# Kernel tuning notes

Measured on AMD Instinct MI355X. Metric: run time of the kernel, lower is better.

The kernel has to match this reference:

```python
import jax, jax.numpy as jnp
import numpy as np

EMBED_DIM = 1024
NUM_HEADS = 16
HEAD_DIM = EMBED_DIM // NUM_HEADS


def setup_inputs() -> dict:
    key = jax.random.key(0)
    ks = jax.random.split(key, 9)
    B, S, D = 2, 2048, EMBED_DIM
    scale = 1.0 / np.sqrt(D)
    inp = {
        "x": jax.random.normal(ks[0], (B, S, D), dtype=jnp.float32),
        "w_q": jax.random.normal(ks[1], (D, D), dtype=jnp.float32) * scale,
        "b_q": jnp.zeros((D,), dtype=jnp.float32),
        "w_k": jax.random.normal(ks[2], (D, D), dtype=jnp.float32) * scale,
        "b_k": jnp.zeros((D,), dtype=jnp.float32),
        "w_v": jax.random.normal(ks[3], (D, D), dtype=jnp.float32) * scale,
        "b_v": jnp.zeros((D,), dtype=jnp.float32),
        "w_o": jax.random.normal(ks[4], (D, D), dtype=jnp.float32) * scale,
        "b_o": jnp.zeros((D,), dtype=jnp.float32),
    }
    return inp


def reference(x, w_q, b_q, w_k, b_k, w_v, b_v, w_o, b_o):
    B, S, D = x.shape
    H, Hd = NUM_HEADS, HEAD_DIM

    def proj(w, b):
        # (B,S,D) @ (D,D) -> (B,S,D) -> (B,H,S,Hd)
        y = jnp.einsum('bsd,df->bsf', x, w) + b
        return y.reshape(B, S, H, Hd).transpose(0, 2, 1, 3)

    q = proj(w_q, b_q)
    k = proj(w_k, b_k)
    v = proj(w_v, b_v)

    scores = jnp.einsum('bhqd,bhkd->bhqk', q, k) / jnp.sqrt(jnp.float32(Hd))
    attn = jax.nn.softmax(scores, axis=-1)
    context = jnp.einsum('bhqk,bhkd->bhqd', attn, v)
    context = context.transpose(0, 2, 1, 3).reshape(B, S, D)
    return jnp.einsum('bsd,df->bsf', context + x, w_o) + b_o
```

## Files before the change

kernel.cpp:

```cpp
#include <hip/hip_runtime.h>
#include <hip/hip_bf16.h>

typedef _Float16 f16;
typedef _Float16 f16x8 __attribute__((ext_vector_type(8)));
typedef _Float16 f16x4 __attribute__((ext_vector_type(4)));
typedef float f32x4 __attribute__((ext_vector_type(4)));

#define EMBED 1024
#define NHEAD 16
#define HDIM 64
#define SEQ 2048
#define BATCH 2
#define NROW (BATCH * SEQ)
#define PSTR 72
#define WBYTES (2 * 64 * PSTR * 2)
#define MBIAS 14.4269504089f
#define QSCALE 0.1803368801f

__device__ __forceinline__ void gld_lds16(const f16* g, f16* l) {
    __builtin_amdgcn_global_load_lds(
        (const __attribute__((address_space(1))) void*)g,
        (__attribute__((address_space(3))) void*)l, 16, 0, 0);
}

__global__ void k_prep(const float* __restrict__ wq, const float* __restrict__ wk,
                       const float* __restrict__ wv, const float* __restrict__ wo,
                       const float* __restrict__ x,
                       f16* __restrict__ wqkvt, f16* __restrict__ wot, f16* __restrict__ xb) {
    if (blockIdx.z >= 4) {
        int i = (((blockIdx.z - 4) * 1024 + blockIdx.y * 32 + blockIdx.x) * 256 + threadIdx.x) * 4;
        float4 v = *(const float4*)&x[i];
        f16x4 o = {(f16)v.x, (f16)v.y, (f16)v.z, (f16)v.w};
        *(f16x4*)&xb[i] = o;
        return;
    }
    const float* W;
    f16* Wt;
    switch (blockIdx.z) {
        case 0: W = wq; Wt = wqkvt; break;
        case 1: W = wk; Wt = wqkvt + 1024 * 1024; break;
        case 2: W = wv; Wt = wqkvt + 2 * 1024 * 1024; break;
        default: W = wo; Wt = wot; break;
    }
    __shared__ float t[32][33];
    int tx = threadIdx.x & 31, ty = threadIdx.x >> 5;
    int r0 = blockIdx.y * 32, c0 = blockIdx.x * 32;
    for (int j = 0; j < 4; ++j)
        t[ty + j * 8][tx] = W[(r0 + ty + j * 8) * 1024 + c0 + tx];
    __syncthreads();
    for (int j = 0; j < 4; ++j)
        Wt[(c0 + ty + j * 8) * 1024 + r0 + tx] = (f16)t[tx][ty + j * 8];
}

__global__ void k_bias(const float* __restrict__ bq, const float* __restrict__ bk,
                       const float* __restrict__ bv, float* __restrict__ bias) {
    int i = blockIdx.x * blockDim.x + threadIdx.x;
    if (i < 3072) bias[i] = (i < 1024) ? bq[i] : ((i < 2048) ? bk[i - 1024] : bv[i - 2048]);
}

template <bool SWAP>
__device__ __forceinline__ void gemm_kloop(const f16* __restrict__ A, const f16* __restrict__ Bt,
                                           int K, f16* Al, f16* Bl, int m0, int n0,
                                           int w, int quad, int l16, int mw, int nw,
                                           int crow, int ccol, f32x4 (&acc)[4][4]) {
    for (int k0 = 0; k0 < K; k0 += 32) {
        __syncthreads();
        gld_lds16(&A[(m0 + crow) * K + k0 + ccol], &Al[(w * 64) * 8]);
        gld_lds16(&A[(m0 + 64 + crow) * K + k0 + ccol], &Al[(256 + w * 64) * 8]);
        gld_lds16(&Bt[(n0 + crow) * K + k0 + ccol], &Bl[(w * 64) * 8]);
        gld_lds16(&Bt[(n0 + 64 + crow) * K + k0 + ccol], &Bl[(256 + w * 64) * 8]);
        __syncthreads();
        f16x8 af[4], bf[4];
        for (int i = 0; i < 4; ++i)
            af[i] = *(const f16x8*)&Al[(mw + i * 16 + l16) * 32 + quad * 8];
        for (int j = 0; j < 4; ++j)
            bf[j] = *(const f16x8*)&Bl[(nw + j * 16 + l16) * 32 + quad * 8];
        for (int i = 0; i < 4; ++i)
            for (int j = 0; j < 4; ++j)
                acc[i][j] = SWAP
                    ? __builtin_amdgcn_mfma_f32_16x16x32_f16(bf[j], af[i], acc[i][j], 0, 0, 0)
                    : __builtin_amdgcn_mfma_f32_16x16x32_f16(af[i], bf[j], acc[i][j], 0, 0, 0);
    }
}

__global__ __launch_bounds__(256) void k_gemm_qkv(const f16* __restrict__ A, const f16* __restrict__ Bt,
                                                  const float* __restrict__ bias,
                                                  f16* __restrict__ qk, f16* __restrict__ Vt) {
    __shared__ __align__(16) f16 Al[128 * 32];
    __shared__ __align__(16) f16 Bl[128 * 32];
    const int K = 1024;
    int tid = threadIdx.x;
    int w = tid >> 6, lane = tid & 63, quad = lane >> 4, l16 = lane & 15;
    int m0 = blockIdx.x * 128, n0 = blockIdx.y * 128;
    int mw = (w >> 1) * 64, nw = (w & 1) * 64;
    int c = w * 64 + lane;
    int crow = c >> 2, ccol = (c & 3) * 8;
    f32x4 acc[4][4] = {};

    if (n0 >= 2048) {
        gemm_kloop<true>(A, Bt, K, Al, Bl, m0, n0, w, quad, l16, mw, nw, crow, ccol, acc);
        for (int i = 0; i < 4; ++i) {
            int mrow = m0 + mw + i * 16 + l16;
            int b = mrow >> 11, s = mrow & 2047;
            for (int j = 0; j < 4; ++j)
                for (int r = 0; r < 4; ++r) {
                    int col = n0 + nw + j * 16 + quad * 4 + r;
                    int d = col - 2048;
                    Vt[(b * 1024 + d) * SEQ + s] = (f16)(acc[i][j][r] + bias[col]);
                }
        }
    } else {
        gemm_kloop<false>(A, Bt, K, Al, Bl, m0, n0, w, quad, l16, mw, nw, crow, ccol, acc);
        for (int i = 0; i < 4; ++i) {
            int row = m0 + mw + i * 16 + quad * 4;
            for (int j = 0; j < 4; ++j) {
                int col = n0 + nw + j * 16 + l16;
                float bval = bias[col];
                for (int r = 0; r < 4; ++r)
                    qk[(row + r) * 2048 + col] = (f16)(acc[i][j][r] + bval);
            }
        }
    }
}

__global__ __launch_bounds__(256) void k_gemm_out(const f16* __restrict__ A, const f16* __restrict__ Bt,
                                                  const float* __restrict__ bias, float* __restrict__ Cout) {
    __shared__ __align__(16) f16 Al[128 * 32];
    __shared__ __align__(16) f16 Bl[64 * 32];
    const int K = 1024, N = 1024;
    int tid = threadIdx.x;
    int w = tid >> 6, lane = tid & 63, quad = lane >> 4, l16 = lane & 15;
    int m0 = blockIdx.x * 128, n0 = blockIdx.y * 64;
    int mw = (w >> 1) * 64, nw = (w & 1) * 32;
    int c = w * 64 + lane;
    int crow = c >> 2, ccol = (c & 3) * 8;
    f32x4 acc[4][2] = {};

    for (int k0 = 0; k0 < K; k0 += 32) {
        __syncthreads();
        gld_lds16(&A[(m0 + crow) * K + k0 + ccol], &Al[(w * 64) * 8]);
        gld_lds16(&A[(m0 + 64 + crow) * K + k0 + ccol], &Al[(256 + w * 64) * 8]);
        gld_lds16(&Bt[(n0 + crow) * K + k0 + ccol], &Bl[(w * 64) * 8]);
        __syncthreads();
        f16x8 af[4], bf[2];
        for (int i = 0; i < 4; ++i)
            af[i] = *(const f16x8*)&Al[(mw + i * 16 + l16) * 32 + quad * 8];
        for (int j = 0; j < 2; ++j)
            bf[j] = *(const f16x8*)&Bl[(nw + j * 16 + l16) * 32 + quad * 8];
        for (int i = 0; i < 4; ++i)
            for (int j = 0; j < 2; ++j)
                acc[i][j] = __builtin_amdgcn_mfma_f32_16x16x32_f16(af[i], bf[j], acc[i][j], 0, 0, 0);
    }

    for (int i = 0; i < 4; ++i) {
        int row = m0 + mw + i * 16 + quad * 4;
        for (int j = 0; j < 2; ++j) {
            int col = n0 + nw + j * 16 + l16;
            float bval = bias[col];
            for (int r = 0; r < 4; ++r)
                Cout[(row + r) * N + col] = acc[i][j][r] + bval;
        }
    }
}

__global__ __launch_bounds__(256, 2) void k_attn(const f16* __restrict__ qk, const f16* __restrict__ Vt,
                                                 const float* __restrict__ x, f16* __restrict__ ctx) {
    __shared__ __align__(16) char smem[4 * WBYTES];

    int tid = threadIdx.x;
    int w = tid >> 6, lane = tid & 63, quad = lane >> 4, l16 = lane & 15;
    int q0 = blockIdx.x * 64;
    int bh = blockIdx.y, b = bh >> 4, h = bh & 15;
    int kbase = 1024 + h * 64;
    int qcol = h * 64;
    int vbase = b * 1024 + h * 64;

    f16* Kw = (f16*)(smem + w * WBYTES);
    f16* Vw = Kw + 64 * PSTR;
    f16* Pw = Kw;

    f16x8 qf[4][2];
    for (int qg = 0; qg < 4; ++qg) {
        int qrow = b * SEQ + q0 + qg * 16 + l16;
        for (int kk = 0; kk < 2; ++kk) {
            f16x8 v = *(const f16x8*)&qk[qrow * 2048 + qcol + kk * 32 + quad * 8];
            for (int e = 0; e < 8; ++e) v[e] = (f16)((float)v[e] * QSCALE);
            qf[qg][kk] = v;
        }
    }

    int srow = lane >> 3;
    int scol = (lane & 7) * 8;
    const f16* kgp = &qk[(b * SEQ + w * 512 + srow) * 2048 + kbase + scol];
    const f16* vgp = &Vt[(vbase + srow) * SEQ + w * 512 + scol];

    f32x4 oacc[4][4] = {};
    float li[4] = {0.f, 0.f, 0.f, 0.f};

    for (int kt = 0; kt < 8; ++kt) {
        f16x8 tk[8], tv[8];
        for (int c = 0; c < 8; ++c) {
            tk[c] = *(const f16x8*)(kgp + c * 8 * 2048);
            tv[c] = *(const f16x8*)(vgp + c * 8 * SEQ);
        }
        kgp += 64 * 2048;
        vgp += 64;
        for (int c = 0; c < 8; ++c) {
            *(f16x8*)&Kw[(c * 8 + srow) * PSTR + scol] = tk[c];
            *(f16x8*)&Vw[(c * 8 + srow) * PSTR + scol] = tv[c];
        }

        f16x8 kf[4][2];
        for (int nt = 0; nt < 4; ++nt)
            for (int kk = 0; kk < 2; ++kk)
                kf[nt][kk] = *(const f16x8*)&Kw[(nt * 16 + l16) * PSTR + kk * 32 + quad * 8];
        asm volatile("s_waitcnt lgkmcnt(0)" ::: "memory");

        for (int qg = 0; qg < 4; ++qg) {
            f32x4 st[4];
            for (int nt = 0; nt < 4; ++nt) {
                f32x4 s = {};
                s = __builtin_amdgcn_mfma_f32_16x16x32_f16(kf[nt][0], qf[qg][0], s, 0, 0, 0);
                s = __builtin_amdgcn_mfma_f32_16x16x32_f16(kf[nt][1], qf[qg][1], s, 0, 0, 0);
                st[nt] = s;
            }
            float rs = 0.f;
            for (int nt = 0; nt < 4; ++nt)
                for (int r = 0; r < 4; ++r) {
                    float p = __builtin_amdgcn_exp2f(st[nt][r] - MBIAS);
                    st[nt][r] = p;
                    rs += p;
                }
            rs += __shfl_xor(rs, 16);
            rs += __shfl_xor(rs, 32);
            li[qg] += rs;
            for (int nt = 0; nt < 4; ++nt) {
                f16x4 pk;
                for (int r = 0; r < 4; ++r) pk[r] = (f16)st[nt][r];
                *(f16x4*)&Pw[(qg * 16 + l16) * PSTR + nt * 16 + quad * 4] = pk;
            }
        }
        asm volatile("s_waitcnt lgkmcnt(0)" ::: "memory");

        f16x8 pf[4][2];
        for (int qg = 0; qg < 4; ++qg)
            for (int kk = 0; kk < 2; ++kk)
                pf[qg][kk] = *(const f16x8*)&Pw[(qg * 16 + l16) * PSTR + kk * 32 + quad * 8];
        for (int nt = 0; nt < 4; ++nt) {
            f16x8 vf0 = *(const f16x8*)&Vw[(nt * 16 + l16) * PSTR + quad * 8];
            f16x8 vf1 = *(const f16x8*)&Vw[(nt * 16 + l16) * PSTR + 32 + quad * 8];
            for (int qg = 0; qg < 4; ++qg) {
                oacc[qg][nt] = __builtin_amdgcn_mfma_f32_16x16x32_f16(pf[qg][0], vf0, oacc[qg][nt], 0, 0, 0);
                oacc[qg][nt] = __builtin_amdgcn_mfma_f32_16x16x32_f16(pf[qg][1], vf1, oacc[qg][nt], 0, 0, 0);
            }
        }
    }

    __syncthreads();
    float* Ow = (float*)(smem + w * WBYTES);
    float* Lw = (float*)(smem + w * WBYTES + 16384);
    for (int qg = 0; qg < 4; ++qg)
        for (int nt = 0; nt < 4; ++nt)
            for (int r = 0; r < 4; ++r)
                Ow[(qg * 16 + quad * 4 + r) * 64 + nt * 16 + l16] = oacc[qg][nt][r];
    if (quad == 0)
        for (int qg = 0; qg < 4; ++qg) Lw[qg * 16 + l16] = li[qg];
    __syncthreads();

    int q = tid >> 2, d0 = (tid & 3) * 16;
    f32x4 a4[4] = {};
    float lsum = 0.f;
    for (int w2 = 0; w2 < 4; ++w2) {
        const float* Ow2 = (const float*)(smem + w2 * WBYTES);
        const float* Lw2 = (const float*)(smem + w2 * WBYTES + 16384);
        for (int j = 0; j < 4; ++j)
            a4[j] += *(const f32x4*)&Ow2[q * 64 + d0 + 4 * j];
        lsum += Lw2[q];
    }
    int g = b * SEQ + q0 + q;
    int cb = h * 64 + d0;
    float inv = 1.f / lsum;
    f16x8 o0, o1;
    for (int j = 0; j < 4; ++j) {
        float4 xv = *(const float4*)&x[g * 1024 + cb + 4 * j];
        float4 r;
        r.x = a4[j][0] * inv + xv.x;
        r.y = a4[j][1] * inv + xv.y;
        r.z = a4[j][2] * inv + xv.z;
        r.w = a4[j][3] * inv + xv.w;
        f16* dst = (j < 2) ? (f16*)&o0 : (f16*)&o1;
        int o = (j & 1) * 4;
        dst[o + 0] = (f16)r.x; dst[o + 1] = (f16)r.y; dst[o + 2] = (f16)r.z; dst[o + 3] = (f16)r.w;
    }
    *(f16x8*)&ctx[g * 1024 + cb] = o0;
    *(f16x8*)&ctx[g * 1024 + cb + 8] = o1;
}

extern "C" void kernel_launch(void* const* d_in, const int* in_sizes, int n_in,
                              void* d_out, int out_size, void* d_ws, size_t ws_size,
                              hipStream_t stream) {
    const float* x  = (const float*)d_in[0];
    const float* wq = (const float*)d_in[1];
    const float* bq = (const float*)d_in[2];
    const float* wk = (const float*)d_in[3];
    const float* bk = (const float*)d_in[4];
    const float* wv = (const float*)d_in[5];
    const float* bv = (const float*)d_in[6];
    const float* wo = (const float*)d_in[7];
    const float* bo = (const float*)d_in[8];
    float* out = (float*)d_out;

    char* ws = (char*)d_ws;
    f16*   xb    = (f16*)(ws);
    f16*   wqkvt = (f16*)(ws + (8u << 20));
    f16*   wot   = (f16*)(ws + (14u << 20));
    float* biasq = (float*)(ws + (16u << 20));
    f16*   qkbuf = (f16*)(ws + (16u << 20) + (64u << 10));
    f16*   vtbuf = (f16*)(ws + (32u << 20) + (64u << 10));
    f16*   ctx   = xb;

    k_prep<<<dim3(32, 32, 8), 256, 0, stream>>>(wq, wk, wv, wo, x, wqkvt, wot, xb);
    k_bias<<<12, 256, 0, stream>>>(bq, bk, bv, biasq);

    k_gemm_qkv<<<dim3(32, 24), 256, 0, stream>>>(xb, wqkvt, biasq, qkbuf, vtbuf);
    k_attn<<<dim3(SEQ / 64, BATCH * NHEAD), 256, 0, stream>>>(qkbuf, vtbuf, x, ctx);
    k_gemm_out<<<dim3(32, 16), 256, 0, stream>>>(ctx, wot, bo, out);
}
```

Baseline: 214.2 us.

## Load K/V MFMA fragments directly from global, shrink LDS, raise occupancy

Stops staging K and V tiles through per-wave LDS buffers and reads the MFMA operand fragments straight from global memory, so LDS holds only the P tile. The smaller LDS footprint lets launch bounds rise from 2 to 4 blocks per CU. The final cross-wave reduction is reworked to fit the smaller buffer: two waves write partial outputs and row sums, then the other two add theirs in after a barrier. Direct fragment loads are less coalesced (16-byte pieces spread across rows) and rely on the cache, and the reduction now needs an extra barrier.

```diff
diff --git a/kernel.cpp b/kernel.cpp
--- a/kernel.cpp
+++ b/kernel.cpp
@@ -13,7 +13,7 @@
 #define BATCH 2
 #define NROW (BATCH * SEQ)
 #define PSTR 72
-#define WBYTES (2 * 64 * PSTR * 2)
+#define PBYTES (64 * PSTR * 2)
 #define MBIAS 14.4269504089f
 #define QSCALE 0.1803368801f
 
@@ -163,9 +163,9 @@
     }
 }
 
-__global__ __launch_bounds__(256, 2) void k_attn(const f16* __restrict__ qk, const f16* __restrict__ Vt,
+__global__ __launch_bounds__(256, 4) void k_attn(const f16* __restrict__ qk, const f16* __restrict__ Vt,
                                                  const float* __restrict__ x, f16* __restrict__ ctx) {
-    __shared__ __align__(16) char smem[4 * WBYTES];
+    __shared__ __align__(16) char smem[4 * PBYTES];
 
     int tid = threadIdx.x;
     int w = tid >> 6, lane = tid & 63, quad = lane >> 4, l16 = lane & 15;
@@ -175,9 +175,7 @@
     int qcol = h * 64;
     int vbase = b * 1024 + h * 64;
 
-    f16* Kw = (f16*)(smem + w * WBYTES);
-    f16* Vw = Kw + 64 * PSTR;
-    f16* Pw = Kw;
+    f16* Pw = (f16*)(smem + w * PBYTES);
 
     f16x8 qf[4][2];
     for (int qg = 0; qg < 4; ++qg) {
@@ -189,32 +187,19 @@
         }
     }
 
-    int srow = lane >> 3;
-    int scol = (lane & 7) * 8;
-    const f16* kgp = &qk[(b * SEQ + w * 512 + srow) * 2048 + kbase + scol];
-    const f16* vgp = &Vt[(vbase + srow) * SEQ + w * 512 + scol];
+    const f16* kfp = &qk[(b * SEQ + w * 512 + l16) * 2048 + kbase + quad * 8];
+    const f16* vfp = &Vt[(vbase + l16) * SEQ + w * 512 + quad * 8];
 
     f32x4 oacc[4][4] = {};
     float li[4] = {0.f, 0.f, 0.f, 0.f};
 
     for (int kt = 0; kt < 8; ++kt) {
-        f16x8 tk[8], tv[8];
-        for (int c = 0; c < 8; ++c) {
-            tk[c] = *(const f16x8*)(kgp + c * 8 * 2048);
-            tv[c] = *(const f16x8*)(vgp + c * 8 * SEQ);
-        }
-        kgp += 64 * 2048;
-        vgp += 64;
-        for (int c = 0; c < 8; ++c) {
-            *(f16x8*)&Kw[(c * 8 + srow) * PSTR + scol] = tk[c];
-            *(f16x8*)&Vw[(c * 8 + srow) * PSTR + scol] = tv[c];
-        }
-
         f16x8 kf[4][2];
-        for (int nt = 0; nt < 4; ++nt)
-            for (int kk = 0; kk < 2; ++kk)
-                kf[nt][kk] = *(const f16x8*)&Kw[(nt * 16 + l16) * PSTR + kk * 32 + quad * 8];
-        asm volatile("s_waitcnt lgkmcnt(0)" ::: "memory");
+        for (int nt = 0; nt < 4; ++nt) {
+            kf[nt][0] = *(const f16x8*)(kfp + nt * 16 * 2048);
+            kf[nt][1] = *(const f16x8*)(kfp + nt * 16 * 2048 + 32);
+        }
+        kfp += 64 * 2048;
 
         for (int qg = 0; qg < 4; ++qg) {
             f32x4 st[4];
@@ -247,36 +232,48 @@
             for (int kk = 0; kk < 2; ++kk)
                 pf[qg][kk] = *(const f16x8*)&Pw[(qg * 16 + l16) * PSTR + kk * 32 + quad * 8];
         for (int nt = 0; nt < 4; ++nt) {
-            f16x8 vf0 = *(const f16x8*)&Vw[(nt * 16 + l16) * PSTR + quad * 8];
-            f16x8 vf1 = *(const f16x8*)&Vw[(nt * 16 + l16) * PSTR + 32 + quad * 8];
+            f16x8 vf0 = *(const f16x8*)(vfp + nt * 16 * SEQ);
+            f16x8 vf1 = *(const f16x8*)(vfp + nt * 16 * SEQ + 32);
             for (int qg = 0; qg < 4; ++qg) {
                 oacc[qg][nt] = __builtin_amdgcn_mfma_f32_16x16x32_f16(pf[qg][0], vf0, oacc[qg][nt], 0, 0, 0);
                 oacc[qg][nt] = __builtin_amdgcn_mfma_f32_16x16x32_f16(pf[qg][1], vf1, oacc[qg][nt], 0, 0, 0);
             }
         }
-    }
-
+        vfp += 64;
+    }
+
+    float* Ow = (float*)(smem + (w & 1) * 16640);
+    float* Lw = (float*)(smem + (w & 1) * 16640 + 16384);
     __syncthreads();
-    float* Ow = (float*)(smem + w * WBYTES);
-    float* Lw = (float*)(smem + w * WBYTES + 16384);
-    for (int qg = 0; qg < 4; ++qg)
-        for (int nt = 0; nt < 4; ++nt)
-            for (int r = 0; r < 4; ++r)
-                Ow[(qg * 16 + quad * 4 + r) * 64 + nt * 16 + l16] = oacc[qg][nt][r];
-    if (quad == 0)
-        for (int qg = 0; qg < 4; ++qg) Lw[qg * 16 + l16] = li[qg];
+    if (w < 2) {
+        for (int qg = 0; qg < 4; ++qg)
+            for (int nt = 0; nt < 4; ++nt)
+                for (int r = 0; r < 4; ++r)
+                    Ow[(qg * 16 + quad * 4 + r) * 64 + nt * 16 + l16] = oacc[qg][nt][r];
+        if (quad == 0)
+            for (int qg = 0; qg < 4; ++qg) Lw[qg * 16 + l16] = li[qg];
+    }
     __syncthreads();
+    if (w >= 2) {
+        for (int qg = 0; qg < 4; ++qg)
+            for (int nt = 0; nt < 4; ++nt)
+                for (int r = 0; r < 4; ++r)
+                    Ow[(qg * 16 + quad * 4 + r) * 64 + nt * 16 + l16] += oacc[qg][nt][r];
+        if (quad == 0)
+            for (int qg = 0; qg < 4; ++qg) Lw[qg * 16 + l16] += li[qg];
+    }
+    __syncthreads();
 
     int q = tid >> 2, d0 = (tid & 3) * 16;
-    f32x4 a4[4] = {};
-    float lsum = 0.f;
-    for (int w2 = 0; w2 < 4; ++w2) {
-        const float* Ow2 = (const float*)(smem + w2 * WBYTES);
-        const float* Lw2 = (const float*)(smem + w2 * WBYTES + 16384);
-        for (int j = 0; j < 4; ++j)
-            a4[j] += *(const f32x4*)&Ow2[q * 64 + d0 + 4 * j];
-        lsum += Lw2[q];
-    }
+    const float* O0 = (const float*)smem;
+    const float* O1 = (const float*)(smem + 16640);
+    f32x4 a4[4];
+    for (int j = 0; j < 4; ++j)
+        a4[j] = *(const f32x4*)&O0[q * 64 + d0 + 4 * j];
+    for (int j = 0; j < 4; ++j)
+        a4[j] += *(const f32x4*)&O1[q * 64 + d0 + 4 * j];
+    float lsum = ((const float*)(smem + 16384))[q] + ((const float*)(smem + 16640 + 16384))[q];
+
     int g = b * SEQ + q0 + q;
     int cb = h * 64 + d0;
     float inv = 1.f / lsum;
```

After: 332.5 us. 55.2% more time.
